# Kernel optimization log

Measured on AMD Instinct MI355X. Metric: run time of the kernel, lower is better.

## Reference

```python
import jax, jax.numpy as jnp
import numpy as np
import math

B, S, D, K = 512, 256, 768, 8  # num_heads = 1, head_size = D
HIST = 256  # hard-coded histogram size in the original module


def setup_inputs() -> dict:
    key = jax.random.key(0)
    ks = jax.random.split(key, 10)
    scale = 0.02
    return {
        "k_in": jax.random.normal(ks[0], (B, S, D), jnp.float32),
        "v_in": jax.random.normal(ks[1], (B, S, D), jnp.float32),
        "q_in": jax.random.normal(ks[2], (B, S, D), jnp.float32),
        "mask": jnp.ones((B, S, S), dtype=bool),
        "Wk": jax.random.normal(ks[3], (D, D), jnp.float32) * scale,
        "bk": jnp.zeros((D,), jnp.float32),
        "Wv": jax.random.normal(ks[4], (D, D), jnp.float32) * scale,
        "bv": jnp.zeros((D,), jnp.float32),
        "Wq": jax.random.normal(ks[5], (D, D), jnp.float32) * scale,
        "bq": jnp.zeros((D,), jnp.float32),
    }


def reference(k_in, v_in, q_in, mask, Wk, bk, Wv, bv, Wq, bq):
    # Linear projections (nn.Linear: x @ W.T + b). num_heads=1 so no head split.
    k = k_in @ Wk.T + bk                      # [B,S,D]
    v = v_in @ Wv.T + bv                      # [B,S,D] (dead code in original, kept for faithfulness)
    q = (q_in @ Wq.T + bq) / math.sqrt(D)     # [B,S,D]

    scores = jnp.einsum("bqd,bkd->bqk", q, k)            # [B,Sq,Sk]
    scores = jnp.where(mask, scores, -jnp.inf)
    attention = jax.nn.softmax(scores, axis=-1)           # dropout = identity (eval)

    # top-k key indices per query row
    _, idx = jax.lax.top_k(attention, K)                  # [B,Sq,K] int32

    # scatter_add histogram: result[b, idx[b,i,j], j] += 1; count[b,c] = sum_j result[b,c,j]
    # => count is simply a per-batch histogram of all Sq*K indices over [0, 256)
    flat = idx.reshape(B, S * K)
    count = jnp.zeros((B, HIST), jnp.float32).at[jnp.arange(B)[:, None], flat].add(1.0)

    _, s_indices = jax.lax.top_k(count, K)                # [B,K]
    return s_indices
```

## Files before the change

kernel.cpp:

```cpp
#include <hip/hip_runtime.h>
#include <cstdint>
#include <cstddef>

#define B_  512
#define S_  256
#define D_  768
#define K_  8
#define HB  256

#define SQRTD_F ((float)27.712812921102035)

__global__ __launch_bounds__(256, 2) void kproj32(
    const float* __restrict__ Xk, const float* __restrict__ Xq,
    const float* __restrict__ Wk, const float* __restrict__ bk,
    const float* __restrict__ Wq, const float* __restrict__ bq,
    float* __restrict__ Kp, float* __restrict__ Qp, int tilesPerInput) {
  __shared__ __align__(16) float Xs[2][8][136];
  __shared__ __align__(16) float Ws[2][8][264];
  int bid = blockIdx.x;
  int divq = 0;
  const float *X, *W, *bias;
  float* P;
  if (bid < tilesPerInput) { X = Xk; W = Wk; bias = bk; P = Kp; }
  else { bid -= tilesPerInput; X = Xq; W = Wq; bias = bq; P = Qp; divq = 1; }
  int mt = bid / 3, nt = bid % 3;
  int m0 = mt * 128, n0 = nt * 256;
  int tid = threadIdx.x;
  int tx = tid & 15, ty = tid >> 4;
  int xr = tid & 127, xq = (tid >> 7) * 4;
  const float* Xp = X + (size_t)(m0 + xr) * D_ + xq;
  const float* Wp = W + (size_t)(n0 + tid) * D_;
  float acc[8][16] = {};
  float4 xa, wa, wb;

  xa = *(const float4*)(Xp);
  wa = *(const float4*)(Wp);
  wb = *(const float4*)(Wp + 4);
  Xs[0][xq + 0][xr] = xa.x; Xs[0][xq + 1][xr] = xa.y;
  Xs[0][xq + 2][xr] = xa.z; Xs[0][xq + 3][xr] = xa.w;
  Ws[0][0][tid] = wa.x; Ws[0][1][tid] = wa.y; Ws[0][2][tid] = wa.z; Ws[0][3][tid] = wa.w;
  Ws[0][4][tid] = wb.x; Ws[0][5][tid] = wb.y; Ws[0][6][tid] = wb.z; Ws[0][7][tid] = wb.w;

  for (int kt = 0; kt < D_; kt += 8) {
    __syncthreads();
    int buf = (kt >> 3) & 1;
    bool pre = (kt + 8) < D_;
    if (pre) {
      xa = *(const float4*)(Xp + kt + 8);
      wa = *(const float4*)(Wp + kt + 8);
      wb = *(const float4*)(Wp + kt + 12);
    }
    #pragma unroll
    for (int kk = 0; kk < 8; ++kk) {
      float xv[8], wv[16];
      *(float4*)(xv)      = *(const float4*)(&Xs[buf][kk][ty * 8]);
      *(float4*)(xv + 4)  = *(const float4*)(&Xs[buf][kk][ty * 8 + 4]);
      *(float4*)(wv)      = *(const float4*)(&Ws[buf][kk][tx * 4]);
      *(float4*)(wv + 4)  = *(const float4*)(&Ws[buf][kk][64 + tx * 4]);
      *(float4*)(wv + 8)  = *(const float4*)(&Ws[buf][kk][128 + tx * 4]);
      *(float4*)(wv + 12) = *(const float4*)(&Ws[buf][kk][192 + tx * 4]);
      #pragma unroll
      for (int i = 0; i < 8; ++i)
        #pragma unroll
        for (int j = 0; j < 16; ++j)
          acc[i][j] = fmaf(xv[i], wv[j], acc[i][j]);
    }
    if (pre) {
      int nb = buf ^ 1;
      Xs[nb][xq + 0][xr] = xa.x; Xs[nb][xq + 1][xr] = xa.y;
      Xs[nb][xq + 2][xr] = xa.z; Xs[nb][xq + 3][xr] = xa.w;
      Ws[nb][0][tid] = wa.x; Ws[nb][1][tid] = wa.y; Ws[nb][2][tid] = wa.z; Ws[nb][3][tid] = wa.w;
      Ws[nb][4][tid] = wb.x; Ws[nb][5][tid] = wb.y; Ws[nb][6][tid] = wb.z; Ws[nb][7][tid] = wb.w;
    }
  }

  #pragma unroll
  for (int i = 0; i < 8; ++i) {
    float* pp = P + (size_t)(m0 + ty * 8 + i) * D_ + n0;
    #pragma unroll
    for (int g = 0; g < 4; ++g) {
      float o[4];
      #pragma unroll
      for (int j = 0; j < 4; ++j) {
        float v = acc[i][g * 4 + j] + bias[n0 + g * 64 + tx * 4 + j];
        if (divq) v = v / SQRTD_F;
        o[j] = v;
      }
      *(float4*)(pp + g * 64 + tx * 4) = *(float4*)(o);
    }
  }
}

__global__ __launch_bounds__(256) void kscore32(
    const float* __restrict__ Qp, const float* __restrict__ Kp,
    int* __restrict__ count, int bBase) {
  __shared__ __align__(16) float Ts[2][16][36];
  __shared__ __align__(16) float Ks[2][16][260];
  __shared__ int hist[256];
  int lb = blockIdx.x / 8, qt = blockIdx.x % 8;
  int b = bBase + lb;
  int tid = threadIdx.x;
  hist[tid] = 0;
  int tx = tid % 32, ty = tid / 32;
  int qr_ = tid / 4, qq = (tid % 4) * 4;
  const float* Qrow = Qp + (size_t)(lb * S_ + qt * 32 + qr_) * D_ + qq;
  const float* Krow = Kp + (size_t)(lb * S_ + tid) * D_;
  float acc[4][8] = {};
  float4 qreg = {0, 0, 0, 0};
  float4 kreg0, kreg1, kreg2, kreg3;

  if (tid < 128) qreg = *(const float4*)(Qrow);
  kreg0 = *(const float4*)(Krow);
  kreg1 = *(const float4*)(Krow + 4);
  kreg2 = *(const float4*)(Krow + 8);
  kreg3 = *(const float4*)(Krow + 12);
  if (tid < 128) {
    Ts[0][qq + 0][qr_] = qreg.x; Ts[0][qq + 1][qr_] = qreg.y;
    Ts[0][qq + 2][qr_] = qreg.z; Ts[0][qq + 3][qr_] = qreg.w;
  }
  {
    Ks[0][ 0][tid] = kreg0.x; Ks[0][ 1][tid] = kreg0.y;
    Ks[0][ 2][tid] = kreg0.z; Ks[0][ 3][tid] = kreg0.w;
    Ks[0][ 4][tid] = kreg1.x; Ks[0][ 5][tid] = kreg1.y;
    Ks[0][ 6][tid] = kreg1.z; Ks[0][ 7][tid] = kreg1.w;
    Ks[0][ 8][tid] = kreg2.x; Ks[0][ 9][tid] = kreg2.y;
    Ks[0][10][tid] = kreg2.z; Ks[0][11][tid] = kreg2.w;
    Ks[0][12][tid] = kreg3.x; Ks[0][13][tid] = kreg3.y;
    Ks[0][14][tid] = kreg3.z; Ks[0][15][tid] = kreg3.w;
  }

  for (int kt = 0; kt < D_; kt += 16) {
    __syncthreads();
    int buf = (kt >> 4) & 1;
    bool pre = (kt + 16) < D_;
    if (pre) {
      if (tid < 128) qreg = *(const float4*)(Qrow + kt + 16);
      kreg0 = *(const float4*)(Krow + kt + 16);
      kreg1 = *(const float4*)(Krow + kt + 20);
      kreg2 = *(const float4*)(Krow + kt + 24);
      kreg3 = *(const float4*)(Krow + kt + 28);
    }
    #pragma unroll
    for (int kk = 0; kk < 16; ++kk) {
      float tv[4], kv[8];
      *(float4*)(tv)     = *(const float4*)(&Ts[buf][kk][ty * 4]);
      *(float4*)(kv)     = *(const float4*)(&Ks[buf][kk][tx * 4]);
      *(float4*)(kv + 4) = *(const float4*)(&Ks[buf][kk][128 + tx * 4]);
      #pragma unroll
      for (int i = 0; i < 4; ++i)
        #pragma unroll
        for (int j = 0; j < 8; ++j)
          acc[i][j] = fmaf(tv[i], kv[j], acc[i][j]);
    }
    if (pre) {
      int nb = buf ^ 1;
      if (tid < 128) {
        Ts[nb][qq + 0][qr_] = qreg.x; Ts[nb][qq + 1][qr_] = qreg.y;
        Ts[nb][qq + 2][qr_] = qreg.z; Ts[nb][qq + 3][qr_] = qreg.w;
      }
      Ks[nb][ 0][tid] = kreg0.x; Ks[nb][ 1][tid] = kreg0.y;
      Ks[nb][ 2][tid] = kreg0.z; Ks[nb][ 3][tid] = kreg0.w;
      Ks[nb][ 4][tid] = kreg1.x; Ks[nb][ 5][tid] = kreg1.y;
      Ks[nb][ 6][tid] = kreg1.z; Ks[nb][ 7][tid] = kreg1.w;
      Ks[nb][ 8][tid] = kreg2.x; Ks[nb][ 9][tid] = kreg2.y;
      Ks[nb][10][tid] = kreg2.z; Ks[nb][11][tid] = kreg2.w;
      Ks[nb][12][tid] = kreg3.x; Ks[nb][13][tid] = kreg3.y;
      Ks[nb][14][tid] = kreg3.z; Ks[nb][15][tid] = kreg3.w;
    }
  }

  for (int i = 0; i < 4; ++i) {
    unsigned live = 0xffu;
    #pragma unroll
    for (int it = 0; it < 8; ++it) {
      float bv = -3.4e38f; int bi = 1 << 30;
      #pragma unroll
      for (int j = 0; j < 8; ++j) {
        if ((live >> j) & 1u) {
          float v = acc[i][j];
          int idx = (j < 4) ? (tx * 4 + j) : (128 + tx * 4 + (j - 4));
          if (v > bv || (v == bv && idx < bi)) { bv = v; bi = idx; }
        }
      }
      #pragma unroll
      for (int off = 1; off < 32; off <<= 1) {
        float ov = __shfl_xor(bv, off);
        int   oi = __shfl_xor(bi, off);
        if (ov > bv || (ov == bv && oi < bi)) { bv = ov; bi = oi; }
      }
      int owner, jj;
      if (bi < 128) { owner = bi >> 2; jj = bi & 3; }
      else          { owner = (bi - 128) >> 2; jj = 4 + ((bi - 128) & 3); }
      if (tx == owner) live &= ~(1u << jj);
      if (tx == 0) atomicAdd(&hist[bi], 1);
    }
  }
  __syncthreads();
  if (hist[tid] > 0) atomicAdd(&count[(size_t)b * HB + tid], hist[tid]);
}

__global__ __launch_bounds__(64) void kfinal(const int* __restrict__ count, int* __restrict__ out) {
  int b = blockIdx.x;
  int lane = threadIdx.x;
  int c[4];
  #pragma unroll
  for (int j = 0; j < 4; ++j) c[j] = count[(size_t)b * HB + lane + 64 * j];
  #pragma unroll
  for (int it = 0; it < 8; ++it) {
    int bk = -0x7fffffff;
    #pragma unroll
    for (int j = 0; j < 4; ++j) {
      int idx = lane + 64 * j;
      int key = c[j] * 256 + (255 - idx);
      if (key > bk) bk = key;
    }
    #pragma unroll
    for (int off = 1; off < 64; off <<= 1) {
      int ok = __shfl_xor(bk, off);
      if (ok > bk) bk = ok;
    }
    int idx = 255 - (bk & 255);
    if (lane == (idx & 63)) c[idx >> 6] = -1;
    if (lane == 0) out[b * K_ + it] = idx;
  }
}

extern "C" void kernel_launch(void* const* d_in, const int* in_sizes, int n_in,
                              void* d_out, int out_size, void* d_ws, size_t ws_size,
                              hipStream_t stream) {
  const float* k_in = (const float*)d_in[0];
  const float* q_in = (const float*)d_in[2];
  const float* Wk   = (const float*)d_in[4];
  const float* bk   = (const float*)d_in[5];
  const float* Wq   = (const float*)d_in[8];
  const float* bq   = (const float*)d_in[9];

  char* ws = (char*)d_ws;
  int* cnt = (int*)ws;
  const size_t offQ = 524288;

  int CB = 64;
  while (CB > 1 && offQ + 2 * (size_t)CB * S_ * D_ * 4 > ws_size) CB >>= 1;
  const int nchunks = B_ / CB;
  float* Qp = (float*)(ws + offQ);
  float* Kp = Qp + (size_t)CB * S_ * D_;

  hipMemsetAsync(cnt, 0, (size_t)B_ * HB * 4, stream);

  for (int c = 0; c < nchunks; ++c) {
    const float* kc = k_in + (size_t)c * CB * S_ * D_;
    const float* qc = q_in + (size_t)c * CB * S_ * D_;
    kproj32<<<CB * 12, 256, 0, stream>>>(kc, qc, Wk, bk, Wq, bq, Kp, Qp, CB * 6);
    kscore32<<<CB * 8, 256, 0, stream>>>(Qp, Kp, cnt, c * CB);
  }
  kfinal<<<B_, 64, 0, stream>>>(cnt, (int*)d_out);
}
```

Measured before the change: 4.659 ms.

## Fuse projection of next chunk with scoring of previous chunk via double buffering

Splits the projection and scoring kernels into device bodies and adds a fused kernel. In each launch, some blocks project chunk c while the rest score chunk c-1, using double-buffered Q/K workspaces. This software-pipelines the two stages so both run inside one launch. It removes per-chunk serialization and launch tail idle time, but needs twice the workspace, which may shrink the chunk size. The scoring kernel also changes to launch bounds of 2 blocks per SM with a shared union buffer.

```diff
diff --git a/kernel.cpp b/kernel.cpp
--- a/kernel.cpp
+++ b/kernel.cpp
@@ -10,14 +10,16 @@
 
 #define SQRTD_F ((float)27.712812921102035)
 
-__global__ __launch_bounds__(256, 2) void kproj32(
+#define SMEM_BYTES 38912
+
+__device__ __forceinline__ void proj_body(
+    char* smem, int bid,
     const float* __restrict__ Xk, const float* __restrict__ Xq,
     const float* __restrict__ Wk, const float* __restrict__ bk,
     const float* __restrict__ Wq, const float* __restrict__ bq,
     float* __restrict__ Kp, float* __restrict__ Qp, int tilesPerInput) {
-  __shared__ __align__(16) float Xs[2][8][136];
-  __shared__ __align__(16) float Ws[2][8][264];
-  int bid = blockIdx.x;
+  float (*Xs)[8][136] = (float (*)[8][136])(smem);
+  float (*Ws)[8][264] = (float (*)[8][264])(smem + 8704);
   int divq = 0;
   const float *X, *W, *bias;
   float* P;
@@ -91,13 +93,14 @@
   }
 }
 
-__global__ __launch_bounds__(256) void kscore32(
+__device__ __forceinline__ void score_body(
+    char* smem, int sbid,
     const float* __restrict__ Qp, const float* __restrict__ Kp,
     int* __restrict__ count, int bBase) {
-  __shared__ __align__(16) float Ts[2][16][36];
-  __shared__ __align__(16) float Ks[2][16][260];
-  __shared__ int hist[256];
-  int lb = blockIdx.x / 8, qt = blockIdx.x % 8;
+  float (*Ts)[16][36]  = (float (*)[16][36])(smem);
+  float (*Ks)[16][260] = (float (*)[16][260])(smem + 4608);
+  int* hist = (int*)(smem + 37888);
+  int lb = sbid / 8, qt = sbid % 8;
   int b = bBase + lb;
   int tid = threadIdx.x;
   hist[tid] = 0;
@@ -199,6 +202,37 @@
   if (hist[tid] > 0) atomicAdd(&count[(size_t)b * HB + tid], hist[tid]);
 }
 
+__global__ __launch_bounds__(256, 2) void kproj32(
+    const float* __restrict__ Xk, const float* __restrict__ Xq,
+    const float* __restrict__ Wk, const float* __restrict__ bk,
+    const float* __restrict__ Wq, const float* __restrict__ bq,
+    float* __restrict__ Kp, float* __restrict__ Qp, int tilesPerInput) {
+  __shared__ __align__(16) char smem[25600];
+  proj_body(smem, blockIdx.x, Xk, Xq, Wk, bk, Wq, bq, Kp, Qp, tilesPerInput);
+}
+
+__global__ __launch_bounds__(256, 2) void kscore32(
+    const float* __restrict__ Qp, const float* __restrict__ Kp,
+    int* __restrict__ count, int bBase) {
+  __shared__ __align__(16) char smem[SMEM_BYTES];
+  score_body(smem, blockIdx.x, Qp, Kp, count, bBase);
+}
+
+__global__ __launch_bounds__(256, 2) void kfused(
+    const float* __restrict__ Xk, const float* __restrict__ Xq,
+    const float* __restrict__ Wk, const float* __restrict__ bk,
+    const float* __restrict__ Wq, const float* __restrict__ bq,
+    float* __restrict__ Kp, float* __restrict__ Qp, int tilesPerInput, int nProjBlocks,
+    const float* __restrict__ Qs, const float* __restrict__ Ks,
+    int* __restrict__ count, int bBase) {
+  __shared__ __align__(16) char smem[SMEM_BYTES];
+  int bid = blockIdx.x;
+  if (bid < nProjBlocks)
+    proj_body(smem, bid, Xk, Xq, Wk, bk, Wq, bq, Kp, Qp, tilesPerInput);
+  else
+    score_body(smem, bid - nProjBlocks, Qs, Ks, count, bBase);
+}
+
 __global__ __launch_bounds__(64) void kfinal(const int* __restrict__ count, int* __restrict__ out) {
   int b = blockIdx.x;
   int lane = threadIdx.x;
@@ -240,18 +274,29 @@
   const size_t offQ = 524288;
 
   int CB = 64;
-  while (CB > 1 && offQ + 2 * (size_t)CB * S_ * D_ * 4 > ws_size) CB >>= 1;
+  while (CB > 1 && offQ + 4ULL * CB * S_ * D_ * 4 > ws_size) CB >>= 1;
   const int nchunks = B_ / CB;
-  float* Qp = (float*)(ws + offQ);
-  float* Kp = Qp + (size_t)CB * S_ * D_;
+  const size_t bufElems = (size_t)CB * S_ * D_;
+  float* base = (float*)(ws + offQ);
+  float* QpB[2] = { base,                base + 2 * bufElems };
+  float* KpB[2] = { base + bufElems,     base + 3 * bufElems };
 
   hipMemsetAsync(cnt, 0, (size_t)B_ * HB * 4, stream);
 
   for (int c = 0; c < nchunks; ++c) {
+    int par = c & 1;
     const float* kc = k_in + (size_t)c * CB * S_ * D_;
     const float* qc = q_in + (size_t)c * CB * S_ * D_;
-    kproj32<<<CB * 12, 256, 0, stream>>>(kc, qc, Wk, bk, Wq, bq, Kp, Qp, CB * 6);
-    kscore32<<<CB * 8, 256, 0, stream>>>(Qp, Kp, cnt, c * CB);
-  }
+    if (c == 0) {
+      kproj32<<<CB * 12, 256, 0, stream>>>(kc, qc, Wk, bk, Wq, bq,
+                                           KpB[0], QpB[0], CB * 6);
+    } else {
+      kfused<<<CB * 12 + CB * 8, 256, 0, stream>>>(
+          kc, qc, Wk, bk, Wq, bq, KpB[par], QpB[par], CB * 6, CB * 12,
+          QpB[par ^ 1], KpB[par ^ 1], cnt, (c - 1) * CB);
+    }
+  }
+  kscore32<<<CB * 8, 256, 0, stream>>>(QpB[(nchunks - 1) & 1], KpB[(nchunks - 1) & 1],
+                                       cnt, (nchunks - 1) * CB);
   kfinal<<<B_, 64, 0, stream>>>(cnt, (int*)d_out);
 }
```

Measured after the change: 4.726 ms. About the same (+1.4%).
